# Performance work log

Measured on AMD Instinct MI355X. Metric: run time of the kernel, lower is better.

The kernel has to match this reference:

```python
import jax, jax.numpy as jnp
import numpy as np

N, E, S, TS = 12, 7, 1024, 3          # num_boxes, edge_types, state_dim, time_step
D_IN = 1056 * 1 * 5 * 5               # emb_features * continuous_frames * crop_size^2


def _gru(x, h0, Wih, Whh, bih, bhh):
    """PyTorch-order GRU (gates r,z,n) over leading time axis. x: [T, B, S]."""
    def step(h, xt):
        gi = xt @ Wih.T + bih
        gh = h @ Whh.T + bhh
        ir, iz, inn = jnp.split(gi, 3, axis=-1)
        hr, hz, hn = jnp.split(gh, 3, axis=-1)
        r = jax.nn.sigmoid(ir + hr)
        z = jax.nn.sigmoid(iz + hz)
        n = jnp.tanh(inn + r * hn)
        h_new = (1.0 - z) * n + z * h
        return h_new, h_new
    _, ys = jax.lax.scan(step, h0, x)
    return ys


def _forward(pose_features, Wc, bc, We, be, Wcomp, bcomp, Wr, br, Wz, bz, Wh, bh,
             Wih, Whh, bih, bhh, Wa, ba):
    B, T = pose_features.shape[:2]
    BT, BNN = B * T, B * N * N
    # compress_fc: [BT, N, D_IN] -> [BT, N, S]
    prop = pose_features.reshape(BT, N, D_IN) @ Wc.T + bc
    # torch code xavier-normal-inits the GRU h0 each call; we use deterministic keys.
    h0_std = (2.0 / (BNN * S + S)) ** 0.5
    base = jax.random.key(42)
    gs = None
    for t in range(TS + 1):
        # all edge_fcs at once: [BT, N, E, S]
        msgs = jnp.einsum('bnd,esd->bnes', prop, We) + be
        msg_flat = msgs.reshape(BT, N * E, S)       # index n*E+e, matches torch cat+view
        scs = []
        for e in range(E):
            rf = msgs[:, :, e, :]                   # [BT, N, S]
            pair = jnp.concatenate([
                jnp.broadcast_to(rf[:, :, None, :], (BT, N, N, S)),
                jnp.broadcast_to(rf[:, None, :, :], (BT, N, N, S))], axis=-1)
            # -> [T, B*N*N, 2S] (permute(1,0,2,3,4) in torch)
            pair = pair.reshape(B, T, N, N, 2 * S).transpose(1, 0, 2, 3, 4).reshape(T, BNN, 2 * S)
            x = pair @ Wcomp.T + bcomp              # compress: [T, BNN, S]
            h0 = jax.random.normal(jax.random.fold_in(base, t * E + e), (BNN, S), dtype=x.dtype) * h0_std
            y = _gru(x, h0, Wih, Whh, bih, bhh)     # [T, BNN, S]
            y = y.reshape(T, B, N, N, S).transpose(1, 0, 2, 3, 4).reshape(BT, N, N, S)
            # edge attention (Dropout is identity in eval): sigmoid(linear->1)
            scs.append(jax.nn.sigmoid(jnp.einsum('bmns,s->bmn', y, Wa[e]) + ba[e]))
        gs = jnp.stack(scs, axis=-1)                # [BT, N, N, E]
        merged = jnp.einsum('bnm,bms->bns', gs.reshape(BT, N, N * E), msg_flat)
        a = jnp.concatenate([merged, prop], axis=-1)
        r = jax.nn.sigmoid(a @ Wr.T + br)
        z = jax.nn.sigmoid(a @ Wz.T + bz)
        h_hat = jnp.tanh(jnp.concatenate([merged, r * prop], axis=-1) @ Wh.T + bh)
        prop = (1.0 - z) * prop + z * h_hat
    box_states = gs                                 # last graph_scores
    action_score = ((1.0 - box_states[..., :1]) * box_states).sum(axis=2).reshape(B, T, N, E)
    actor_score = (1.0 - box_states[..., 0]).reshape(B, T, N, N)
    acty_score = jax.nn.softmax(
        (action_score * actor_score.sum(axis=-1)[..., None]).sum(axis=2)[:, :, 1:], axis=-1)
    return action_score, acty_score, actor_score


def setup_inputs() -> dict:
    key = jax.random.key(0)
    ks = jax.random.split(key, 16)
    B, T = 2, 4
    k = 1.0 / np.sqrt(S)  # torch GRU default uniform init bound
    return {
        'pose_features': jax.random.normal(ks[0], (B, T, N, D_IN), jnp.float32),
        'boxes_in': jax.random.uniform(ks[1], (B, T, N, 4), jnp.float32),
        'boxes_dhdw': jax.random.normal(ks[2], (B, T, N, 2), jnp.float32),
        'bboxes_num_in': jax.random.randint(ks[3], (B, T), 1, N),
        'actor_label': jax.random.randint(ks[4], (B, T, N), 0, E),
        'Wc': 0.01 * jax.random.normal(ks[5], (S, D_IN), jnp.float32),
        'bc': jnp.zeros((S,), jnp.float32),
        'We': 0.01 * jax.random.normal(ks[6], (E, S, S), jnp.float32),
        'be': jnp.zeros((E, S), jnp.float32),
        'Wcomp': 0.01 * jax.random.normal(ks[7], (S, 2 * S), jnp.float32),
        'bcomp': jnp.zeros((S,), jnp.float32),
        'Wr': 0.01 * jax.random.normal(ks[8], (S, 2 * S), jnp.float32),
        'br': jnp.zeros((S,), jnp.float32),
        'Wz': 0.01 * jax.random.normal(ks[9], (S, 2 * S), jnp.float32),
        'bz': jnp.zeros((S,), jnp.float32),
        'Wh': 0.01 * jax.random.normal(ks[10], (S, 2 * S), jnp.float32),
        'bh': jnp.zeros((S,), jnp.float32),
        'Wih': jax.random.uniform(ks[11], (3 * S, S), jnp.float32, -k, k),
        'Whh': jax.random.uniform(ks[12], (3 * S, S), jnp.float32, -k, k),
        'bih': jax.random.uniform(ks[13], (3 * S,), jnp.float32, -k, k),
        'bhh': jax.random.uniform(ks[14], (3 * S,), jnp.float32, -k, k),
        'Wa': 0.01 * jax.random.normal(ks[15], (E, S), jnp.float32),
        'ba': jnp.zeros((E,), jnp.float32),
    }


def reference(pose_features, boxes_in, boxes_dhdw, bboxes_num_in, actor_label,
              Wc, bc, We, be, Wcomp, bcomp, Wr, br, Wz, bz, Wh, bh,
              Wih, Whh, bih, bhh, Wa, ba):
    # boxes_in / boxes_dhdw / bboxes_num_in / actor_label only provide shapes in eval mode
    del boxes_in, boxes_dhdw, bboxes_num_in, actor_label
    return _forward(pose_features, Wc, bc, We, be, Wcomp, bcomp, Wr, br, Wz, bz,
                    Wh, bh, Wih, Whh, bih, bhh, Wa, ba)
```

## Files before the change

kernel.cpp:

```cpp
#include <hip/hip_runtime.h>
#include <math.h>

#define NQ 12
#define EQ 7
#define SQ 1024
#define TSQ 3
#define DIN 26400
#define BQ 2
#define TQ 4
#define BT 8
#define BNN 288
#define NROWS 2016
#define G3S 3072
#define BK 32

typedef unsigned short u16;
typedef float f32x4 __attribute__((ext_vector_type(4)));
typedef short s16x8 __attribute__((ext_vector_type(8)));

__device__ __forceinline__ short bh(float f) {
    unsigned u = __float_as_uint(f);
    return (short)((u + 0x8000u) >> 16);
}
__device__ __forceinline__ float b2f(u16 u) {
    return __uint_as_float((unsigned)u << 16);
}
__device__ __forceinline__ s16x8 pack8(float4 a, float4 b) {
    s16x8 r;
    r[0] = bh(a.x); r[1] = bh(a.y); r[2] = bh(a.z); r[3] = bh(a.w);
    r[4] = bh(b.x); r[5] = bh(b.y); r[6] = bh(b.z); r[7] = bh(b.w);
    return r;
}
__device__ __forceinline__ void gload16(const void* g, void* l) {
    __builtin_amdgcn_global_load_lds(
        (const __attribute__((address_space(1))) unsigned*)g,
        (__attribute__((address_space(3))) unsigned*)l, 16, 0, 0);
}
__device__ inline float sigmoidf(float x) { return 1.f / (1.f + expf(-x)); }

template<int AS32, int BS32>
__global__ __launch_bounds__(256)
void gemm_mfma(const void* __restrict__ Ap, long sAb, int lda,
               const void* __restrict__ Bp, long sBb, int ldb,
               const float* __restrict__ bias, long sBiasb,
               float* __restrict__ C, long sCb, int ldc,
               u16* __restrict__ Cb, long sCbb, int ldcb,
               int M, int Nn, int K, int act, int ksplit)
{
    __shared__ __align__(16) u16 lA[2][256][8];
    __shared__ __align__(16) u16 lB[2][512][8];

    const int z = blockIdx.z;
    const int az = z / ksplit;
    const int ks = z - az * ksplit;
    const int Ksl = K / ksplit;
    const int kbase = ks * Ksl;

    const char* Abase = (const char*)Ap + (long)az * sAb * (AS32 ? 4 : 2);
    const char* Bbase = (const char*)Bp + (long)az * sBb * (BS32 ? 4 : 2);

    const int tid = threadIdx.x;
    const int lane = tid & 63;
    const int wave = tid >> 6;
    const int row0 = blockIdx.x * 64;
    const int col0 = blockIdx.y * 128;
    const int wcol = wave * 32;

    const int akg = tid >> 6;
    long arow = row0 + (tid & 63); if (arow >= M) arow = M - 1;
    const int bkg0 = tid >> 7;
    const int s1 = tid + 256;
    const int bkg1 = s1 >> 7;
    long brow0 = col0 + (tid & 127); if (brow0 >= Nn) brow0 = Nn - 1;
    long brow1 = col0 + (s1 & 127);  if (brow1 >= Nn) brow1 = Nn - 1;

    const int arw32 = tid >> 2, akg32 = tid & 3;
    long ar32 = row0 + arw32; if (ar32 >= M) ar32 = M - 1;
    const int brw32 = tid >> 1, bh32 = tid & 1;
    long br32 = col0 + brw32; if (br32 >= Nn) br32 = Nn - 1;

    f32x4 acc[4][2] = {};

#define STAGE(b, kt) do {                                                     \
    const int k0_ = kbase + (kt) * BK;                                        \
    if constexpr (AS32) {                                                     \
        const float* A32 = (const float*)Abase;                               \
        const float* p0 = A32 + ar32 * lda + k0_ + akg32 * 8;                 \
        *(s16x8*)&lA[b][akg32 * 64 + arw32][0] =                              \
            pack8(*(const float4*)p0, *(const float4*)(p0 + 4));              \
    } else {                                                                  \
        const u16* A16 = (const u16*)Abase;                                   \
        gload16(A16 + arow * lda + k0_ + akg * 8, &lA[b][tid][0]);            \
    }                                                                         \
    if constexpr (BS32) {                                                     \
        const float* B32 = (const float*)Bbase;                               \
        const float* q0 = B32 + br32 * ldb + k0_ + bh32 * 16;                 \
        *(s16x8*)&lB[b][(bh32 * 2) * 128 + brw32][0] =                        \
            pack8(*(const float4*)q0, *(const float4*)(q0 + 4));              \
        *(s16x8*)&lB[b][(bh32 * 2 + 1) * 128 + brw32][0] =                    \
            pack8(*(const float4*)(q0 + 8), *(const float4*)(q0 + 12));       \
    } else {                                                                  \
        const u16* B16 = (const u16*)Bbase;                                   \
        gload16(B16 + brow0 * ldb + k0_ + bkg0 * 8, &lB[b][tid][0]);          \
        gload16(B16 + brow1 * ldb + k0_ + bkg1 * 8, &lB[b][s1][0]);           \
    }                                                                         \
} while (0)

    const int nk = Ksl / BK;
    STAGE(0, 0);
    __syncthreads();
    int buf = 0;
    const int kg = lane >> 4;
    const int lr = lane & 15;
    for (int kt = 0; kt < nk; ++kt) {
        if (kt + 1 < nk) STAGE(buf ^ 1, kt + 1);
        s16x8 af[4], bfr[2];
#pragma unroll
        for (int m = 0; m < 4; ++m)
            af[m] = *(const s16x8*)&lA[buf][kg * 64 + m * 16 + lr][0];
#pragma unroll
        for (int n = 0; n < 2; ++n)
            bfr[n] = *(const s16x8*)&lB[buf][kg * 128 + wcol + n * 16 + lr][0];
#pragma unroll
        for (int m = 0; m < 4; ++m)
#pragma unroll
            for (int n = 0; n < 2; ++n)
                acc[m][n] = __builtin_amdgcn_mfma_f32_16x16x32_bf16(af[m], bfr[n], acc[m][n], 0, 0, 0);
        __syncthreads();
        buf ^= 1;
    }
#undef STAGE

    const int ccol = lane & 15;
    const int crow = (lane >> 4) * 4;
#pragma unroll
    for (int n = 0; n < 2; ++n) {
        const int c = col0 + wcol + n * 16 + ccol;
        const float bv = bias ? bias[(long)az * sBiasb + c] : 0.f;
#pragma unroll
        for (int m = 0; m < 4; ++m) {
            const int rb = row0 + m * 16 + crow;
#pragma unroll
            for (int q = 0; q < 4; ++q) {
                const int r = rb + q;
                if (r >= M) continue;
                float v = acc[m][n][q] + bv;
                if (act == 1) v = 1.f / (1.f + expf(-v));
                else if (act == 2) v = tanhf(v);
                if (C)  C[(long)z * sCb + (long)r * ldc + c] = v;
                if (Cb) Cb[(long)z * sCbb + (long)r * ldcb + c] = (u16)bh(v);
            }
        }
    }
}

__global__ __launch_bounds__(256)
void gemm128_f32(const float* __restrict__ A, int lda,
                 const float* __restrict__ Bm, int ldb,
                 float* __restrict__ C, long sCb, int ldc,
                 u16* __restrict__ Cb, int ldcb,
                 int M, int Nn, int K, int ksplit)
{
    __shared__ __align__(16) u16 lA[2][512][8];
    __shared__ __align__(16) u16 lB[2][512][8];

    const int ks = blockIdx.z;
    const int Ksl = K / ksplit;
    const int kbase = ks * Ksl;

    const int tid = threadIdx.x;
    const int lane = tid & 63;
    const int wave = tid >> 6;
    const int row0 = blockIdx.x * 128;
    const int col0 = blockIdx.y * 128;
    const int wrow = (wave >> 1) * 64;
    const int wcol = (wave & 1) * 64;

    const int rw = tid >> 1, hf = tid & 1;
    long ar = row0 + rw; if (ar >= M) ar = M - 1;
    long br = col0 + rw; if (br >= Nn) br = Nn - 1;

    f32x4 acc[4][4] = {};

#define STAGE128(b, kt) do {                                                  \
    const int k0_ = kbase + (kt) * BK;                                        \
    const float* p = A + ar * lda + k0_ + hf * 16;                            \
    *(s16x8*)&lA[b][(hf * 2) * 128 + rw][0] =                                 \
        pack8(*(const float4*)p, *(const float4*)(p + 4));                    \
    *(s16x8*)&lA[b][(hf * 2 + 1) * 128 + rw][0] =                             \
        pack8(*(const float4*)(p + 8), *(const float4*)(p + 12));             \
    const float* q = Bm + br * ldb + k0_ + hf * 16;                           \
    *(s16x8*)&lB[b][(hf * 2) * 128 + rw][0] =                                 \
        pack8(*(const float4*)q, *(const float4*)(q + 4));                    \
    *(s16x8*)&lB[b][(hf * 2 + 1) * 128 + rw][0] =                             \
        pack8(*(const float4*)(q + 8), *(const float4*)(q + 12));             \
} while (0)

    const int nk = Ksl / BK;
    STAGE128(0, 0);
    __syncthreads();
    int buf = 0;
    const int kg = lane >> 4;
    const int lr = lane & 15;
    for (int kt = 0; kt < nk; ++kt) {
        if (kt + 1 < nk) STAGE128(buf ^ 1, kt + 1);
        s16x8 af[4], bfr[4];
#pragma unroll
        for (int m = 0; m < 4; ++m)
            af[m] = *(const s16x8*)&lA[buf][kg * 128 + wrow + m * 16 + lr][0];
#pragma unroll
        for (int n = 0; n < 4; ++n)
            bfr[n] = *(const s16x8*)&lB[buf][kg * 128 + wcol + n * 16 + lr][0];
#pragma unroll
        for (int m = 0; m < 4; ++m)
#pragma unroll
            for (int n = 0; n < 4; ++n)
                acc[m][n] = __builtin_amdgcn_mfma_f32_16x16x32_bf16(af[m], bfr[n], acc[m][n], 0, 0, 0);
        __syncthreads();
        buf ^= 1;
    }
#undef STAGE128

    const int ccol = lane & 15;
    const int crow = (lane >> 4) * 4;
#pragma unroll
    for (int n = 0; n < 4; ++n) {
        const int c = col0 + wcol + n * 16 + ccol;
#pragma unroll
        for (int m = 0; m < 4; ++m) {
            const int rb = row0 + wrow + m * 16 + crow;
#pragma unroll
            for (int q = 0; q < 4; ++q) {
                const int r = rb + q;
                if (r >= M) continue;
                float v = acc[m][n][q];
                if (C)  C[(long)ks * sCb + (long)r * ldc + c] = v;
                if (Cb) Cb[(long)r * ldcb + c] = (u16)bh(v);
            }
        }
    }
}

__global__ __launch_bounds__(256)
void gh_gru(const u16* __restrict__ hb_in, const u16* __restrict__ Whh_b,
            const float* __restrict__ bhh, const float* __restrict__ Gnm,
            const float* __restrict__ cbias,
            float* __restrict__ h, u16* __restrict__ hb_out,
            const float* __restrict__ Wa, float* __restrict__ gs_part, int tt)
{
    __shared__ __align__(16) u16 lA[2][512][8];
    __shared__ __align__(16) u16 lB[2][1536][8];
    __shared__ float rowdot[64];

    const int f = blockIdx.x;
    const int ly = 2 * (f & 7) + ((f >> 3) & 1);
    const int lx = f >> 4;
    const int row0 = lx * 64;
    const int col0 = ly * 64;

    const int tid = threadIdx.x;
    const int lane = tid & 63;
    const int wave = tid >> 6;
    const int wr = wave >> 1;
    const int wc = wave & 1;

    long arow = row0 + (tid & 63); if (arow >= NROWS) arow = NROWS - 1;

    const u16* aP0 = hb_in + arow * SQ + (tid >> 6) * 8;
    const u16* aP1 = aP0 + 32;
    const u16* bP[6];
#pragma unroll
    for (int j = 0; j < 6; ++j) {
        const int s = tid + j * 256;
        const int bk16 = s / 192;
        const int grow = s - bk16 * 192;
        bP[j] = Whh_b + (long)((grow >> 6) * SQ + col0 + (grow & 63)) * SQ + bk16 * 8;
    }

    f32x4 acc[3][2][2] = {};

#define GSTAGE(b, kt) do {                                                    \
    const int k0_ = (kt) * 64;                                                \
    gload16(aP0 + k0_, &lA[b][tid][0]);                                       \
    gload16(aP1 + k0_, &lA[b][tid + 256][0]);                                 \
    _Pragma("unroll")                                                         \
    for (int j = 0; j < 6; ++j)                                               \
        gload16(bP[j] + k0_, &lB[b][tid + j * 256][0]);                       \
} while (0)

    GSTAGE(0, 0);
    __syncthreads();
    int buf = 0;
    const int kg = lane >> 4;
    const int lr = lane & 15;
    for (int kt = 0; kt < 16; ++kt) {
        if (kt + 1 < 16) GSTAGE(buf ^ 1, kt + 1);
#pragma unroll
        for (int kk = 0; kk < 2; ++kk) {
            const int k16 = kk * 4 + kg;
            s16x8 af[2], bfr[3][2];
#pragma unroll
            for (int m = 0; m < 2; ++m)
                af[m] = *(const s16x8*)&lA[buf][k16 * 64 + wr * 32 + m * 16 + lr][0];
#pragma unroll
            for (int g = 0; g < 3; ++g)
#pragma unroll
                for (int n = 0; n < 2; ++n)
                    bfr[g][n] = *(const s16x8*)&lB[buf][k16 * 192 + g * 64 + wc * 32 + n * 16 + lr][0];
#pragma unroll
            for (int g = 0; g < 3; ++g)
#pragma unroll
                for (int m = 0; m < 2; ++m)
#pragma unroll
                    for (int n = 0; n < 2; ++n)
                        acc[g][m][n] = __builtin_amdgcn_mfma_f32_16x16x32_bf16(af[m], bfr[g][n], acc[g][m][n], 0, 0, 0);
        }
        __syncthreads();
        buf ^= 1;
    }
#undef GSTAGE

    if (tid < 64) rowdot[tid] = 0.f;
    __syncthreads();

    const int ccol = lane & 15;
    const int crow4 = (lane >> 4) * 4;
    int col2[2];
    float cbv[3][2], bhv[3][2];
#pragma unroll
    for (int n = 0; n < 2; ++n) {
        const int c = col0 + wc * 32 + n * 16 + ccol;
        col2[n] = c;
#pragma unroll
        for (int g = 0; g < 3; ++g) {
            cbv[g][n] = cbias[g * SQ + c];
            bhv[g][n] = bhh[g * SQ + c];
        }
    }

#pragma unroll
    for (int m = 0; m < 2; ++m) {
#pragma unroll
        for (int q = 0; q < 4; ++q) {
            const int row = row0 + wr * 32 + m * 16 + crow4 + q;
            const bool valid = (row < NROWS);
            float d = 0.f;
            if (valid) {
                const int e = row / BNN;
                const int rr = row - e * BNN;
                const int b_ = rr / 144;
                const int ni = (rr / 12) % 12;
                const int mi = rr % 12;
                const int bt = b_ * TQ + tt;
                const float* gnp = Gnm + ((long)e * 96 + bt * 12 + ni) * 6144;
                const float* gmp = Gnm + ((long)e * 96 + bt * 12 + mi) * 6144 + G3S;
                const float* wap = Wa + (long)e * SQ;
#pragma unroll
                for (int n = 0; n < 2; ++n) {
                    const int c = col2[n];
                    float gr  = acc[0][m][n][q] + bhv[0][n] + gnp[c] + gmp[c] + cbv[0][n];
                    float gz  = acc[1][m][n][q] + bhv[1][n] + gnp[SQ + c] + gmp[SQ + c] + cbv[1][n];
                    float ghn = acc[2][m][n][q] + bhv[2][n];
                    float gin = gnp[2 * SQ + c] + gmp[2 * SQ + c] + cbv[2][n];
                    float rg = sigmoidf(gr);
                    float zg = sigmoidf(gz);
                    float nn2 = tanhf(gin + rg * ghn);
                    float hp = h[(long)row * SQ + c];
                    float hn = (1.f - zg) * nn2 + zg * hp;
                    h[(long)row * SQ + c] = hn;
                    hb_out[(long)row * SQ + c] = (u16)bh(hn);
                    d += hn * wap[c];
                }
            }
            d += __shfl_xor(d, 1); d += __shfl_xor(d, 2);
            d += __shfl_xor(d, 4); d += __shfl_xor(d, 8);
            if (valid && ccol == 0)
                atomicAdd(&rowdot[wr * 32 + m * 16 + crow4 + q], d);
        }
    }
    __syncthreads();
    if (tid < 64) {
        const int row = row0 + tid;
        if (row < NROWS) gs_part[((long)tt * 2048 + row) * 16 + ly] = rowdot[tid];
    }
}

__global__ __launch_bounds__(256)
void gru0(const float* __restrict__ Gnm, const float* __restrict__ cbias,
          const float* __restrict__ bhh,
          float* __restrict__ h, u16* __restrict__ hb_out,
          const float* __restrict__ Wa, const float* __restrict__ ba,
          float* __restrict__ gs)
{
    const int row = blockIdx.x;
    const int e = row / BNN;
    const int r = row % BNN;
    const int b_ = r / 144;
    const int ni = (r / 12) % 12;
    const int mi = r % 12;
    const int bt = b_ * TQ;

    const float* gnp = Gnm + ((long)e * 96 + bt * 12 + ni) * 6144;
    const float* gmp = Gnm + ((long)e * 96 + bt * 12 + mi) * 6144 + G3S;
    float* hp = h + (long)row * SQ;
    u16* hpb = hb_out + (long)row * SQ;

    const int s = threadIdx.x * 4;

    float4 gnR = *(const float4*)(gnp + s);
    float4 gnZ = *(const float4*)(gnp + SQ + s);
    float4 gnN = *(const float4*)(gnp + 2 * SQ + s);
    float4 gmR = *(const float4*)(gmp + s);
    float4 gmZ = *(const float4*)(gmp + SQ + s);
    float4 gmN = *(const float4*)(gmp + 2 * SQ + s);
    float4 cbR = *(const float4*)(cbias + s);
    float4 cbZ = *(const float4*)(cbias + SQ + s);
    float4 cbN = *(const float4*)(cbias + 2 * SQ + s);
    float4 bhR = *(const float4*)(bhh + s);
    float4 bhZ = *(const float4*)(bhh + SQ + s);
    float4 bhN = *(const float4*)(bhh + 2 * SQ + s);
    float4 wv  = *(const float4*)(Wa + (long)e * SQ + s);

    float4 hn4;
    float dot = 0.f;

#define GRU0_COMP(c)                                                \
    {                                                               \
        float rg = sigmoidf(gnR.c + gmR.c + cbR.c + bhR.c);         \
        float zg = sigmoidf(gnZ.c + gmZ.c + cbZ.c + bhZ.c);         \
        float nn = tanhf(gnN.c + gmN.c + cbN.c + rg * bhN.c);       \
        float hn = (1.f - zg) * nn;                                 \
        hn4.c = hn;                                                 \
        dot += hn * wv.c;                                           \
    }
    GRU0_COMP(x) GRU0_COMP(y) GRU0_COMP(z) GRU0_COMP(w)
#undef GRU0_COMP

    *(float4*)(hp + s) = hn4;
    ushort4 hb4;
    hb4.x = (u16)bh(hn4.x); hb4.y = (u16)bh(hn4.y);
    hb4.z = (u16)bh(hn4.z); hb4.w = (u16)bh(hn4.w);
    *(ushort4*)(hpb + s) = hb4;

    for (int off = 32; off > 0; off >>= 1) dot += __shfl_down(dot, off);
    __shared__ float red[4];
    if ((threadIdx.x & 63) == 0) red[threadIdx.x >> 6] = dot;
    __syncthreads();
    if (threadIdx.x == 0) {
        float tot = red[0] + red[1] + red[2] + red[3] + ba[e];
        gs[((bt * 12 + ni) * 12 + mi) * EQ + e] = sigmoidf(tot);
    }
}

__global__ void gs_fin_all(const float* __restrict__ gs_part, const float* __restrict__ ba,
                           float* __restrict__ gs)
{
    int idx = blockIdx.x * 256 + threadIdx.x;
    if (idx >= 3 * 2048) return;
    const int tt = 1 + (idx >> 11);
    const int row = idx & 2047;
    if (row >= NROWS) return;
    float s = 0.f;
#pragma unroll
    for (int j = 0; j < 16; ++j) s += gs_part[((long)tt * 2048 + row) * 16 + j];
    const int e = row / BNN;
    const int rr = row - e * BNN;
    const int b_ = rr / 144;
    const int ni = (rr / 12) % 12;
    const int mi = rr % 12;
    const int bt = b_ * TQ + tt;
    gs[((bt * 12 + ni) * 12 + mi) * EQ + e] = sigmoidf(s + ba[e]);
}

__global__ __launch_bounds__(256)
void reduce_k(const float* __restrict__ part, int ksplit, int mn, int Nn,
              const float* __restrict__ bias, long sBiasB, int act,
              float* __restrict__ Cf, long sCfB, int ldcf,
              u16* __restrict__ Cb, long sCbB, int ldcb)
{
    int i4 = blockIdx.x * 256 + threadIdx.x;
    int total4 = mn >> 2;
    if (i4 >= total4) return;
    int b = blockIdx.y;
    const float4* p4 = (const float4*)part;
    float4 s = make_float4(0.f, 0.f, 0.f, 0.f);
    for (int ks = 0; ks < ksplit; ++ks) {
        float4 v = p4[(long)(b * ksplit + ks) * total4 + i4];
        s.x += v.x; s.y += v.y; s.z += v.z; s.w += v.w;
    }
    int i = i4 << 2;
    int r = i / Nn, c = i % Nn;
    if (bias) {
        float4 bv = *(const float4*)(bias + (long)b * sBiasB + c);
        s.x += bv.x; s.y += bv.y; s.z += bv.z; s.w += bv.w;
    }
    if (act == 1) {
        s.x = sigmoidf(s.x); s.y = sigmoidf(s.y); s.z = sigmoidf(s.z); s.w = sigmoidf(s.w);
    } else if (act == 2) {
        s.x = tanhf(s.x); s.y = tanhf(s.y); s.z = tanhf(s.z); s.w = tanhf(s.w);
    }
    if (Cf) *(float4*)(Cf + (long)b * sCfB + (long)r * ldcf + c) = s;
    if (Cb) {
        ushort4 o;
        o.x = (u16)bh(s.x); o.y = (u16)bh(s.y); o.z = (u16)bh(s.z); o.w = (u16)bh(s.w);
        *(ushort4*)(Cb + (long)b * sCbB + (long)r * ldcb + c) = o;
    }
}

__global__ void cvt_bf16_k(const float* __restrict__ src, u16* __restrict__ dst, int n4)
{
    int i = blockIdx.x * 256 + threadIdx.x;
    if (i >= n4) return;
    float4 v = ((const float4*)src)[i];
    ushort4 o;
    o.x = (u16)bh(v.x); o.y = (u16)bh(v.y); o.z = (u16)bh(v.z); o.w = (u16)bh(v.w);
    ((ushort4*)dst)[i] = o;
}

__global__ __launch_bounds__(256)
void transpose_wc(const float* __restrict__ Wcomp, float* __restrict__ W1T, float* __restrict__ W2T)
{
    __shared__ float t1[32][33];
    __shared__ float t2[32][33];
    const int tx = threadIdx.x & 31;
    const int ty = threadIdx.x >> 5;
    const int d0 = blockIdx.x * 32;
    const int s0 = blockIdx.y * 32;
#pragma unroll
    for (int k = 0; k < 4; ++k) {
        int d = d0 + ty + k * 8;
        t1[ty + k * 8][tx] = Wcomp[(long)d * 2048 + s0 + tx];
        t2[ty + k * 8][tx] = Wcomp[(long)d * 2048 + 1024 + s0 + tx];
    }
    __syncthreads();
#pragma unroll
    for (int k = 0; k < 4; ++k) {
        int s = s0 + ty + k * 8;
        W1T[(long)s * 1024 + d0 + tx] = t1[tx][ty + k * 8];
        W2T[(long)s * 1024 + d0 + tx] = t2[tx][ty + k * 8];
    }
}

__global__ void pack_rz(const float* __restrict__ Wr, const float* __restrict__ Wz,
                        const float* __restrict__ br, const float* __restrict__ bz,
                        u16* __restrict__ Wrz, float* __restrict__ brz)
{
    int i4 = blockIdx.x * 256 + threadIdx.x;
    if (i4 < 512) {
        int c = i4 * 4;
        float4 b = (c < 1024) ? *(const float4*)(br + c) : *(const float4*)(bz + c - 1024);
        *(float4*)(brz + c) = b;
    }
    if (i4 >= 1048576) return;
    int i = i4 * 4;
    int j = i >> 11;
    int c = i & 2047;
    float4 v = (j < 1024) ? *(const float4*)(Wr + (long)j * 2048 + c)
                          : *(const float4*)(Wz + (long)(j - 1024) * 2048 + c);
    ushort4 o;
    o.x = (u16)bh(v.x); o.y = (u16)bh(v.y); o.z = (u16)bh(v.z); o.w = (u16)bh(v.w);
    *(ushort4*)(Wrz + i) = o;
}

__global__ void cbias_k(const float* __restrict__ Wih, const float* __restrict__ bih,
                        const float* __restrict__ bcomp, float* __restrict__ cbias)
{
    int g = blockIdx.x * blockDim.x + threadIdx.x;
    if (g >= G3S) return;
    const float* w = Wih + (long)g * SQ;
    float s = 0.f;
    for (int k = 0; k < SQ; k += 4) {
        float4 wv = *(const float4*)(w + k);
        float4 bv = *(const float4*)(bcomp + k);
        s += wv.x * bv.x + wv.y * bv.y + wv.z * bv.z + wv.w * bv.w;
    }
    cbias[g] = s + bih[g];
}

__global__ __launch_bounds__(256)
void merged_amat_k(const float* __restrict__ gs, const u16* __restrict__ msgs_b,
                   const float* __restrict__ prop, u16* __restrict__ amat_b)
{
    const int bn = blockIdx.x;
    const int bt = bn / 12;
    __shared__ float g[84];
    if (threadIdx.x < 84) g[threadIdx.x] = gs[bn * 84 + threadIdx.x];
    __syncthreads();
    const int s = threadIdx.x * 4;
    float4 acc = make_float4(0.f, 0.f, 0.f, 0.f);
    for (int j = 0; j < 84; ++j) {
        const ushort4 mv = *(const ushort4*)(msgs_b + ((long)(bt * 84 + j)) * SQ + s);
        float gj = g[j];
        acc.x += gj * b2f(mv.x);
        acc.y += gj * b2f(mv.y);
        acc.z += gj * b2f(mv.z);
        acc.w += gj * b2f(mv.w);
    }
    ushort4 o;
    o.x = (u16)bh(acc.x); o.y = (u16)bh(acc.y); o.z = (u16)bh(acc.z); o.w = (u16)bh(acc.w);
    *(ushort4*)(amat_b + (long)bn * 2048 + s) = o;
    float4 pv = *(const float4*)(prop + (long)bn * SQ + s);
    ushort4 o2;
    o2.x = (u16)bh(pv.x); o2.y = (u16)bh(pv.y); o2.z = (u16)bh(pv.z); o2.w = (u16)bh(pv.w);
    *(ushort4*)(amat_b + (long)bn * 2048 + 1024 + s) = o2;
}

__global__ void ahat_k(const float* __restrict__ rz, const float* __restrict__ prop,
                       u16* __restrict__ amat_b)
{
    int i = blockIdx.x * 256 + threadIdx.x;
    int rrow = i >> 10, c = i & 1023;
    float r = rz[(long)rrow * 2048 + c];
    amat_b[(long)rrow * 2048 + 1024 + c] = (u16)bh(r * prop[i]);
}

__global__ void propupd_k(const float* __restrict__ rz, const float* __restrict__ hhat,
                          float* __restrict__ prop, u16* __restrict__ prop_b)
{
    int i = blockIdx.x * 256 + threadIdx.x;
    int rrow = i >> 10, c = i & 1023;
    float z = rz[(long)rrow * 2048 + 1024 + c];
    float v = (1.f - z) * prop[i] + z * hhat[i];
    prop[i] = v;
    prop_b[i] = (u16)bh(v);
}

__global__ __launch_bounds__(256)
void outputs_k(const float* __restrict__ gs, float* __restrict__ out)
{
    __shared__ float s_act[672];
    __shared__ float s_asum[96];
    int tid = threadIdx.x;
    for (int idx = tid; idx < 672; idx += 256) {
        int bn = idx / 7, e = idx % 7;
        float sum = 0.f;
        for (int m = 0; m < 12; ++m) {
            float g0 = gs[bn * 84 + m * 7];
            sum += (1.f - g0) * gs[bn * 84 + m * 7 + e];
        }
        s_act[idx] = sum;
        out[idx] = sum;
    }
    for (int idx = tid; idx < 96; idx += 256) {
        float a = 0.f;
        for (int m = 0; m < 12; ++m) a += 1.f - gs[idx * 84 + m * 7];
        s_asum[idx] = a;
    }
    for (int idx = tid; idx < 1152; idx += 256) {
        int bn = idx / 12, m = idx % 12;
        out[720 + idx] = 1.f - gs[bn * 84 + m * 7];
    }
    __syncthreads();
    if (tid < 8) {
        float tmp[6];
        float mx = -1e30f;
        for (int e = 1; e < 7; ++e) {
            float sum = 0.f;
            for (int n = 0; n < 12; ++n) {
                int bn = tid * 12 + n;
                sum += s_act[bn * 7 + e] * s_asum[bn];
            }
            tmp[e - 1] = sum;
            mx = fmaxf(mx, sum);
        }
        float den = 0.f;
        for (int e = 0; e < 6; ++e) { tmp[e] = expf(tmp[e] - mx); den += tmp[e]; }
        for (int e = 0; e < 6; ++e) out[672 + tid * 6 + e] = tmp[e] / den;
    }
}

template<int AS32, int BS32>
static void launch_gemm(const void* A, long sAb, int lda,
                        const void* B, long sBb, int ldb,
                        const float* bias, long sBiasb,
                        float* C, long sCb, int ldc,
                        u16* Cb, long sCbb, int ldcb,
                        int M, int Nn, int K, int act, int batch, int ksplit,
                        hipStream_t stream)
{
    dim3 grid((M + 63) / 64, (Nn + 127) / 128, batch * ksplit);
    gemm_mfma<AS32, BS32><<<grid, dim3(256), 0, stream>>>(
        A, sAb, lda, B, sBb, ldb, bias, sBiasb, C, sCb, ldc, Cb, sCbb, ldcb,
        M, Nn, K, act, ksplit);
}

extern "C" void kernel_launch(void* const* d_in, const int* in_sizes, int n_in,
                              void* d_out, int out_size, void* d_ws, size_t ws_size,
                              hipStream_t stream)
{
    const float* pose  = (const float*)d_in[0];
    const float* Wc    = (const float*)d_in[5];
    const float* bc    = (const float*)d_in[6];
    const float* We    = (const float*)d_in[7];
    const float* be    = (const float*)d_in[8];
    const float* Wcomp = (const float*)d_in[9];
    const float* bcomp = (const float*)d_in[10];
    const float* Wr    = (const float*)d_in[11];
    const float* br    = (const float*)d_in[12];
    const float* Wz    = (const float*)d_in[13];
    const float* bz    = (const float*)d_in[14];
    const float* Wh    = (const float*)d_in[15];
    const float* bh_   = (const float*)d_in[16];
    const float* Wih   = (const float*)d_in[17];
    const float* Whh   = (const float*)d_in[18];
    const float* bih   = (const float*)d_in[19];
    const float* bhh   = (const float*)d_in[20];
    const float* Wa    = (const float*)d_in[21];
    const float* ba    = (const float*)d_in[22];

    float* ws = (float*)d_ws;
    float* prop    = ws;
    float* cbias   = prop + 98304;
    float* h       = cbias + 3072;
    float* Gnm     = h + 2064384;
    float* scratch = Gnm + 4128768;
    float* gs      = scratch + 8257536;
    float* rz      = gs + 8064;
    float* hhat    = rz + 196608;
    float* brz     = hhat + 98304;
    float* gs_part = brz + 2048;
    float* fend    = gs_part + 131072;
    u16* Whh_b  = (u16*)fend;
    u16* Wnm_b  = Whh_b + 3145728;
    u16* Wrz_b  = Wnm_b + 6291456;
    u16* msgs_b = Wrz_b + 4194304;
    u16* h_b0   = msgs_b + 688128;
    u16* h_b1   = h_b0 + 2064384;
    u16* prop_b = h_b1 + 2064384;
    u16* amat_b = prop_b + 98304;

    float* W1T = scratch;
    float* W2T = scratch + 1048576;

    hipLaunchKernelGGL(cvt_bf16_k, dim3(3072), dim3(256), 0, stream, Whh, Whh_b, 786432);
    hipLaunchKernelGGL(cbias_k, dim3(12), dim3(256), 0, stream, Wih, bih, bcomp, cbias);
    hipLaunchKernelGGL(transpose_wc, dim3(32, 32), dim3(256), 0, stream, Wcomp, W1T, W2T);
    hipLaunchKernelGGL(pack_rz, dim3(4096), dim3(256), 0, stream, Wr, Wz, br, bz, Wrz_b, brz);
    gemm128_f32<<<dim3(24, 8, 1), dim3(256), 0, stream>>>(
        Wih, SQ, W1T, SQ, nullptr, 0, SQ, Wnm_b, SQ, G3S, SQ, SQ, 1);
    gemm128_f32<<<dim3(24, 8, 1), dim3(256), 0, stream>>>(
        Wih, SQ, W2T, SQ, nullptr, 0, SQ, Wnm_b + (long)G3S * SQ, SQ, G3S, SQ, SQ, 1);
    gemm128_f32<<<dim3(1, 8, 75), dim3(256), 0, stream>>>(
        pose, DIN, Wc, DIN, scratch, 98304, SQ, nullptr, SQ, 96, SQ, DIN, 75);
    hipLaunchKernelGGL(reduce_k, dim3(96, 1), dim3(256), 0, stream,
                       scratch, 75, 98304, SQ, bc, 0L, 0,
                       prop, 0L, SQ, prop_b, 0L, SQ);

    for (int t = 0; t <= TSQ; ++t) {
        launch_gemm<0, 1>(prop_b, 0, SQ, We, (long)SQ * SQ, SQ, nullptr, 0,
                          scratch, 98304, SQ, nullptr, 0, 0, 96, SQ, SQ, 0, EQ, 4, stream);
        hipLaunchKernelGGL(reduce_k, dim3(96, EQ), dim3(256), 0, stream,
                           scratch, 4, 98304, SQ, be, (long)SQ, 0,
                           (float*)nullptr, 0L, 0, msgs_b, (long)SQ, EQ * SQ);
        launch_gemm<0, 0>(msgs_b, SQ, EQ * SQ, Wnm_b, 0, SQ, nullptr, 0,
                          Gnm, 589824, 6 * SQ, nullptr, 0, 0, 96, 6 * SQ, SQ, 0, EQ, 1, stream);
        hipLaunchKernelGGL(gru0, dim3(NROWS), dim3(256), 0, stream,
                           Gnm, cbias, bhh, h, h_b0, Wa, ba, gs);
        for (int tt = 1; tt < TQ; ++tt) {
            const u16* hin = (tt & 1) ? h_b0 : h_b1;
            u16* hout = (tt & 1) ? h_b1 : h_b0;
            hipLaunchKernelGGL(gh_gru, dim3(512), dim3(256), 0, stream,
                               hin, Whh_b, bhh, Gnm, cbias, h, hout, Wa, gs_part, tt);
        }
        hipLaunchKernelGGL(gs_fin_all, dim3(24), dim3(256), 0, stream, gs_part, ba, gs);
        if (t < TSQ) {
            hipLaunchKernelGGL(merged_amat_k, dim3(96), dim3(256), 0, stream,
                               gs, msgs_b, prop, amat_b);
            launch_gemm<0, 0>(amat_b, 0, 2 * SQ, Wrz_b, 0, 2 * SQ, nullptr, 0,
                              scratch, 196608, 2 * SQ, nullptr, 0, 0, 96, 2 * SQ, 2 * SQ, 0, 1, 8, stream);
            hipLaunchKernelGGL(reduce_k, dim3(192, 1), dim3(256), 0, stream,
                               scratch, 8, 196608, 2 * SQ, brz, 0L, 1,
                               rz, 0L, 2 * SQ, (u16*)nullptr, 0L, 0);
            hipLaunchKernelGGL(ahat_k, dim3(384), dim3(256), 0, stream, rz, prop, amat_b);
            launch_gemm<0, 1>(amat_b, 0, 2 * SQ, Wh, 0, 2 * SQ, nullptr, 0,
                              scratch, 98304, SQ, nullptr, 0, 0, 96, SQ, 2 * SQ, 0, 1, 8, stream);
            hipLaunchKernelGGL(reduce_k, dim3(96, 1), dim3(256), 0, stream,
                               scratch, 8, 98304, SQ, bh_, 0L, 2,
                               hhat, 0L, SQ, (u16*)nullptr, 0L, 0);
            hipLaunchKernelGGL(propupd_k, dim3(384), dim3(256), 0, stream, rz, hhat, prop, prop_b);
        }
    }

    hipLaunchKernelGGL(outputs_k, dim3(1), dim3(256), 0, stream, gs, (float*)d_out);
}
```

Measured before the change: 1.252 ms.

## Store Gnm in bf16, widen gh_gru tiles, use bf16 MFMA for compress GEMM

The GRU input-gate projection Gnm is now written and read as bf16 instead of fp32, halving its memory traffic in gru0 and gh_gru. gh_gru moves to 512-thread blocks covering 128 rows each, which halves the grid and the number of times each Whh tile is reloaded. The large compress_fc GEMM now converts pose and Wc to bf16 and uses the bf16 MFMA path with a different split-K factor instead of the fp32 GEMM. The cost is lower precision in the gate inputs and in prop, plus extra conversion kernels for pose and the 27M-element Wc on every call.

```diff
diff --git a/kernel.cpp b/kernel.cpp
--- a/kernel.cpp
+++ b/kernel.cpp
@@ -241,21 +241,21 @@
     }
 }
 
-__global__ __launch_bounds__(256)
+__global__ __launch_bounds__(512)
 void gh_gru(const u16* __restrict__ hb_in, const u16* __restrict__ Whh_b,
-            const float* __restrict__ bhh, const float* __restrict__ Gnm,
+            const float* __restrict__ bhh, const u16* __restrict__ Gnm_b,
             const float* __restrict__ cbias,
             float* __restrict__ h, u16* __restrict__ hb_out,
             const float* __restrict__ Wa, float* __restrict__ gs_part, int tt)
 {
-    __shared__ __align__(16) u16 lA[2][512][8];
+    __shared__ __align__(16) u16 lA[2][1024][8];
     __shared__ __align__(16) u16 lB[2][1536][8];
-    __shared__ float rowdot[64];
+    __shared__ float rowdot[128];
 
     const int f = blockIdx.x;
     const int ly = 2 * (f & 7) + ((f >> 3) & 1);
     const int lx = f >> 4;
-    const int row0 = lx * 64;
+    const int row0 = lx * 128;
     const int col0 = ly * 64;
 
     const int tid = threadIdx.x;
@@ -264,14 +264,14 @@
     const int wr = wave >> 1;
     const int wc = wave & 1;
 
-    long arow = row0 + (tid & 63); if (arow >= NROWS) arow = NROWS - 1;
-
-    const u16* aP0 = hb_in + arow * SQ + (tid >> 6) * 8;
+    long arow = row0 + (tid & 127); if (arow >= NROWS) arow = NROWS - 1;
+
+    const u16* aP0 = hb_in + arow * SQ + (tid >> 7) * 8;
     const u16* aP1 = aP0 + 32;
-    const u16* bP[6];
-#pragma unroll
-    for (int j = 0; j < 6; ++j) {
-        const int s = tid + j * 256;
+    const u16* bP[3];
+#pragma unroll
+    for (int j = 0; j < 3; ++j) {
+        const int s = tid + j * 512;
         const int bk16 = s / 192;
         const int grow = s - bk16 * 192;
         bP[j] = Whh_b + (long)((grow >> 6) * SQ + col0 + (grow & 63)) * SQ + bk16 * 8;
@@ -282,10 +282,10 @@
 #define GSTAGE(b, kt) do {                                                    \
     const int k0_ = (kt) * 64;                                                \
     gload16(aP0 + k0_, &lA[b][tid][0]);                                       \
-    gload16(aP1 + k0_, &lA[b][tid + 256][0]);                                 \
+    gload16(aP1 + k0_, &lA[b][tid + 512][0]);                                 \
     _Pragma("unroll")                                                         \
-    for (int j = 0; j < 6; ++j)                                               \
-        gload16(bP[j] + k0_, &lB[b][tid + j * 256][0]);                       \
+    for (int j = 0; j < 3; ++j)                                               \
+        gload16(bP[j] + k0_, &lB[b][tid + j * 512][0]);                       \
 } while (0)
 
     GSTAGE(0, 0);
@@ -301,7 +301,7 @@
             s16x8 af[2], bfr[3][2];
 #pragma unroll
             for (int m = 0; m < 2; ++m)
-                af[m] = *(const s16x8*)&lA[buf][k16 * 64 + wr * 32 + m * 16 + lr][0];
+                af[m] = *(const s16x8*)&lA[buf][k16 * 128 + wr * 32 + m * 16 + lr][0];
 #pragma unroll
             for (int g = 0; g < 3; ++g)
 #pragma unroll
@@ -320,7 +320,7 @@
     }
 #undef GSTAGE
 
-    if (tid < 64) rowdot[tid] = 0.f;
+    if (tid < 128) rowdot[tid] = 0.f;
     __syncthreads();
 
     const int ccol = lane & 15;
@@ -352,16 +352,16 @@
                 const int ni = (rr / 12) % 12;
                 const int mi = rr % 12;
                 const int bt = b_ * TQ + tt;
-                const float* gnp = Gnm + ((long)e * 96 + bt * 12 + ni) * 6144;
-                const float* gmp = Gnm + ((long)e * 96 + bt * 12 + mi) * 6144 + G3S;
+                const u16* gnp = Gnm_b + ((long)e * 96 + bt * 12 + ni) * 6144;
+                const u16* gmp = Gnm_b + ((long)e * 96 + bt * 12 + mi) * 6144 + G3S;
                 const float* wap = Wa + (long)e * SQ;
 #pragma unroll
                 for (int n = 0; n < 2; ++n) {
                     const int c = col2[n];
-                    float gr  = acc[0][m][n][q] + bhv[0][n] + gnp[c] + gmp[c] + cbv[0][n];
-                    float gz  = acc[1][m][n][q] + bhv[1][n] + gnp[SQ + c] + gmp[SQ + c] + cbv[1][n];
+                    float gr  = acc[0][m][n][q] + bhv[0][n] + b2f(gnp[c]) + b2f(gmp[c]) + cbv[0][n];
+                    float gz  = acc[1][m][n][q] + bhv[1][n] + b2f(gnp[SQ + c]) + b2f(gmp[SQ + c]) + cbv[1][n];
                     float ghn = acc[2][m][n][q] + bhv[2][n];
-                    float gin = gnp[2 * SQ + c] + gmp[2 * SQ + c] + cbv[2][n];
+                    float gin = b2f(gnp[2 * SQ + c]) + b2f(gmp[2 * SQ + c]) + cbv[2][n];
                     float rg = sigmoidf(gr);
                     float zg = sigmoidf(gz);
                     float nn2 = tanhf(gin + rg * ghn);
@@ -379,14 +379,14 @@
         }
     }
     __syncthreads();
-    if (tid < 64) {
+    if (tid < 128) {
         const int row = row0 + tid;
         if (row < NROWS) gs_part[((long)tt * 2048 + row) * 16 + ly] = rowdot[tid];
     }
 }
 
 __global__ __launch_bounds__(256)
-void gru0(const float* __restrict__ Gnm, const float* __restrict__ cbias,
+void gru0(const u16* __restrict__ Gnm_b, const float* __restrict__ cbias,
           const float* __restrict__ bhh,
           float* __restrict__ h, u16* __restrict__ hb_out,
           const float* __restrict__ Wa, const float* __restrict__ ba,
@@ -400,19 +400,19 @@
     const int mi = r % 12;
     const int bt = b_ * TQ;
 
-    const float* gnp = Gnm + ((long)e * 96 + bt * 12 + ni) * 6144;
-    const float* gmp = Gnm + ((long)e * 96 + bt * 12 + mi) * 6144 + G3S;
+    const u16* gnp = Gnm_b + ((long)e * 96 + bt * 12 + ni) * 6144;
+    const u16* gmp = Gnm_b + ((long)e * 96 + bt * 12 + mi) * 6144 + G3S;
     float* hp = h + (long)row * SQ;
     u16* hpb = hb_out + (long)row * SQ;
 
     const int s = threadIdx.x * 4;
 
-    float4 gnR = *(const float4*)(gnp + s);
-    float4 gnZ = *(const float4*)(gnp + SQ + s);
-    float4 gnN = *(const float4*)(gnp + 2 * SQ + s);
-    float4 gmR = *(const float4*)(gmp + s);
-    float4 gmZ = *(const float4*)(gmp + SQ + s);
-    float4 gmN = *(const float4*)(gmp + 2 * SQ + s);
+    ushort4 nR = *(const ushort4*)(gnp + s);
+    ushort4 nZ = *(const ushort4*)(gnp + SQ + s);
+    ushort4 nN = *(const ushort4*)(gnp + 2 * SQ + s);
+    ushort4 mR = *(const ushort4*)(gmp + s);
+    ushort4 mZ = *(const ushort4*)(gmp + SQ + s);
+    ushort4 mN = *(const ushort4*)(gmp + 2 * SQ + s);
     float4 cbR = *(const float4*)(cbias + s);
     float4 cbZ = *(const float4*)(cbias + SQ + s);
     float4 cbN = *(const float4*)(cbias + 2 * SQ + s);
@@ -424,16 +424,16 @@
     float4 hn4;
     float dot = 0.f;
 
-#define GRU0_COMP(c)                                                \
-    {                                                               \
-        float rg = sigmoidf(gnR.c + gmR.c + cbR.c + bhR.c);         \
-        float zg = sigmoidf(gnZ.c + gmZ.c + cbZ.c + bhZ.c);         \
-        float nn = tanhf(gnN.c + gmN.c + cbN.c + rg * bhN.c);       \
-        float hn = (1.f - zg) * nn;                                 \
-        hn4.c = hn;                                                 \
-        dot += hn * wv.c;                                           \
-    }
-    GRU0_COMP(x) GRU0_COMP(y) GRU0_COMP(z) GRU0_COMP(w)
+#define GRU0_COMP(c, u)                                                       \
+    {                                                                         \
+        float rg = sigmoidf(b2f(nR.u) + b2f(mR.u) + cbR.c + bhR.c);           \
+        float zg = sigmoidf(b2f(nZ.u) + b2f(mZ.u) + cbZ.c + bhZ.c);           \
+        float nn = tanhf(b2f(nN.u) + b2f(mN.u) + cbN.c + rg * bhN.c);         \
+        float hn = (1.f - zg) * nn;                                           \
+        hn4.c = hn;                                                           \
+        dot += hn * wv.c;                                                     \
+    }
+    GRU0_COMP(x, x) GRU0_COMP(y, y) GRU0_COMP(z, z) GRU0_COMP(w, w)
 #undef GRU0_COMP
 
     *(float4*)(hp + s) = hn4;
@@ -712,8 +712,7 @@
     float* prop    = ws;
     float* cbias   = prop + 98304;
     float* h       = cbias + 3072;
-    float* Gnm     = h + 2064384;
-    float* scratch = Gnm + 4128768;
+    float* scratch = h + 2064384;
     float* gs      = scratch + 8257536;
     float* rz      = gs + 8064;
     float* hhat    = rz + 196608;
@@ -723,16 +722,21 @@
     u16* Whh_b  = (u16*)fend;
     u16* Wnm_b  = Whh_b + 3145728;
     u16* Wrz_b  = Wnm_b + 6291456;
-    u16* msgs_b = Wrz_b + 4194304;
+    u16* Gnm_b  = Wrz_b + 4194304;
+    u16* msgs_b = Gnm_b + 4128768;
     u16* h_b0   = msgs_b + 688128;
     u16* h_b1   = h_b0 + 2064384;
     u16* prop_b = h_b1 + 2064384;
     u16* amat_b = prop_b + 98304;
+    u16* pose_b = amat_b + 196608;
+    u16* Wc_b   = pose_b + 2534400;
 
     float* W1T = scratch;
     float* W2T = scratch + 1048576;
 
     hipLaunchKernelGGL(cvt_bf16_k, dim3(3072), dim3(256), 0, stream, Whh, Whh_b, 786432);
+    hipLaunchKernelGGL(cvt_bf16_k, dim3(2475), dim3(256), 0, stream, pose, pose_b, 633600);
+    hipLaunchKernelGGL(cvt_bf16_k, dim3(26400), dim3(256), 0, stream, Wc, Wc_b, 6758400);
     hipLaunchKernelGGL(cbias_k, dim3(12), dim3(256), 0, stream, Wih, bih, bcomp, cbias);
     hipLaunchKernelGGL(transpose_wc, dim3(32, 32), dim3(256), 0, stream, Wcomp, W1T, W2T);
     hipLaunchKernelGGL(pack_rz, dim3(4096), dim3(256), 0, stream, Wr, Wz, br, bz, Wrz_b, brz);
@@ -740,10 +744,10 @@
         Wih, SQ, W1T, SQ, nullptr, 0, SQ, Wnm_b, SQ, G3S, SQ, SQ, 1);
     gemm128_f32<<<dim3(24, 8, 1), dim3(256), 0, stream>>>(
         Wih, SQ, W2T, SQ, nullptr, 0, SQ, Wnm_b + (long)G3S * SQ, SQ, G3S, SQ, SQ, 1);
-    gemm128_f32<<<dim3(1, 8, 75), dim3(256), 0, stream>>>(
-        pose, DIN, Wc, DIN, scratch, 98304, SQ, nullptr, SQ, 96, SQ, DIN, 75);
+    launch_gemm<0, 0>(pose_b, 0, DIN, Wc_b, 0, DIN, nullptr, 0,
+                      scratch, 98304, SQ, nullptr, 0, 0, 96, SQ, DIN, 0, 1, 55, stream);
     hipLaunchKernelGGL(reduce_k, dim3(96, 1), dim3(256), 0, stream,
-                       scratch, 75, 98304, SQ, bc, 0L, 0,
+                       scratch, 55, 98304, SQ, bc, 0L, 0,
                        prop, 0L, SQ, prop_b, 0L, SQ);
 
     for (int t = 0; t <= TSQ; ++t) {
@@ -753,14 +757,14 @@
                            scratch, 4, 98304, SQ, be, (long)SQ, 0,
                            (float*)nullptr, 0L, 0, msgs_b, (long)SQ, EQ * SQ);
         launch_gemm<0, 0>(msgs_b, SQ, EQ * SQ, Wnm_b, 0, SQ, nullptr, 0,
-                          Gnm, 589824, 6 * SQ, nullptr, 0, 0, 96, 6 * SQ, SQ, 0, EQ, 1, stream);
+                          nullptr, 0, 0, Gnm_b, 589824, 6 * SQ, 96, 6 * SQ, SQ, 0, EQ, 1, stream);
         hipLaunchKernelGGL(gru0, dim3(NROWS), dim3(256), 0, stream,
-                           Gnm, cbias, bhh, h, h_b0, Wa, ba, gs);
+                           Gnm_b, cbias, bhh, h, h_b0, Wa, ba, gs);
         for (int tt = 1; tt < TQ; ++tt) {
             const u16* hin = (tt & 1) ? h_b0 : h_b1;
             u16* hout = (tt & 1) ? h_b1 : h_b0;
-            hipLaunchKernelGGL(gh_gru, dim3(512), dim3(256), 0, stream,
-                               hin, Whh_b, bhh, Gnm, cbias, h, hout, Wa, gs_part, tt);
+            hipLaunchKernelGGL(gh_gru, dim3(256), dim3(512), 0, stream,
+                               hin, Whh_b, bhh, Gnm_b, cbias, h, hout, Wa, gs_part, tt);
         }
         hipLaunchKernelGGL(gs_fin_all, dim3(24), dim3(256), 0, stream, gs_part, ba, gs);
         if (t < TSQ) {
```

Measured after the change: 1.181 ms. 1.06x faster.
